# Optimization experiments

Hardware: AMD Instinct MI355X
Metric: run time of the kernel (lower is better)

## Reference

```python
import jax, jax.numpy as jnp
import numpy as np

N = 256   # events in the document
D = 768   # embed_dim
R = 7     # out_dim == num_relations (label 6 == NONE, filtered from graph)
H = 150   # Score hidden_dim


def _pair_idx(n):
    # torch ordering: [(i,k) for i in range(n) for k in range(n) if i != k]
    ii = np.repeat(np.arange(n), n)
    jj = np.tile(np.arange(n), n)
    m = ii != jj
    return jnp.asarray(ii[m], jnp.int32), jnp.asarray(jj[m], jnp.int32)


def _mlp(x, w1, b1, w2, b2, w3, b3):
    # Score module, eval mode (dropout off)
    h = jax.nn.relu(x @ w1 + b1)
    h = jax.nn.relu(h @ w2 + b2)
    return h @ w3 + b3


def _rgcn_conv(x, src, dst, etype, keep, w, root, bias):
    # PyG RGCNConv (num_bases=None, aggr='mean'):
    # out[i] = sum_r mean_{j in N_r(i)} x_j @ W_r + x_i @ root + bias
    # Linearity lets us aggregate x_j first, then apply W_r once per (node, rel).
    n, d = x.shape
    r = w.shape[0]
    seg = dst.astype(jnp.int32) * r + etype.astype(jnp.int32)      # [E]
    msg = x[src] * keep[:, None]                                   # [E, D]
    agg = jax.ops.segment_sum(msg, seg, num_segments=n * r)        # [N*R, D]
    cnt = jax.ops.segment_sum(keep, seg, num_segments=n * r)       # [N*R]
    mean = (agg / jnp.maximum(cnt, 1.0)[:, None]).reshape(n, r, d)
    return jnp.einsum('nrd,rde->ne', mean, w) + x @ root + bias


def setup_inputs():
    key = jax.random.key(0)
    ks = jax.random.split(key, 12)
    g = lambda k, s, sc=0.02: jax.random.normal(k, s, dtype=jnp.float32) * sc
    P = N * (N - 1)
    z = lambda s: jnp.zeros(s, jnp.float32)
    return {
        'embed': jax.random.normal(ks[0], (N, D), dtype=jnp.float32),
        'labels': jax.random.randint(ks[1], (P,), 0, R),
        'conv1_w': g(ks[2], (R, D, D)), 'conv1_root': g(ks[3], (D, D)), 'conv1_bias': z((D,)),
        'conv2_w': g(ks[4], (R, D, D)), 'conv2_root': g(ks[5], (D, D)), 'conv2_bias': z((D,)),
        'base_w1': g(ks[6], (2 * D, H)), 'base_b1': z((H,)),
        'base_w2': g(ks[7], (H, H)), 'base_b2': z((H,)),
        'base_w3': g(ks[8], (H, R)), 'base_b3': z((R,)),
        'cls_w1': g(ks[9], (2 * D, H)), 'cls_b1': z((H,)),
        'cls_w2': g(ks[10], (H, H)), 'cls_b2': z((H,)),
        'cls_w3': g(ks[11], (H, R)), 'cls_b3': z((R,)),
    }


def reference(embed, labels, conv1_w, conv1_root, conv1_bias,
              conv2_w, conv2_root, conv2_bias,
              base_w1, base_b1, base_w2, base_b2, base_w3, base_b3,
              cls_w1, cls_b1, cls_w2, cls_b2, cls_w3, cls_b3):
    n = embed.shape[0]
    src, dst = _pair_idx(n)                                        # all ordered pairs i != k

    # baseline scorer on raw-embedding pairs (frozen in torch; its argmax is unused)
    pairs0 = jnp.concatenate([embed[src], embed[dst]], axis=1)     # [P, 2D]
    _noise = _mlp(pairs0, base_w1, base_b1, base_w2, base_b2, base_w3, base_b3)

    # graph edges: keep only pairs whose label != 6 (NONE)
    keep = (labels != R - 1).astype(embed.dtype)                   # [P]
    etype = jnp.where(labels == R - 1, 0, labels)                  # dummy type, zero-weighted

    # RGCN (eval mode: dropout off)
    x = jax.nn.relu(_rgcn_conv(embed, src, dst, etype, keep, conv1_w, conv1_root, conv1_bias))
    out = _rgcn_conv(x, src, dst, etype, keep, conv2_w, conv2_root, conv2_bias)

    # classifier on RGCN-output pairs (full pair set again)
    pairs = jnp.concatenate([out[src], out[dst]], axis=1)          # [P, 2D]
    return _mlp(pairs, cls_w1, cls_b1, cls_w2, cls_b2, cls_w3, cls_b3)  # [P, 7]
```

## Files before the change

kernel.cpp:

```cpp
#include <hip/hip_runtime.h>

typedef unsigned short u16;
typedef unsigned int   u32;
typedef __attribute__((ext_vector_type(8))) short bf16x8;
typedef __attribute__((ext_vector_type(4))) float f32x4;

#define KCAT 5376

struct Params {
    const float* embed; const int* labels;
    const float* c1w; const float* c1root; const float* c1b;
    const float* c2w; const float* c2root; const float* c2b;
    const float* cw1; const float* cb1; const float* cw2;
    const float* cb2; const float* cw3; const float* cb3;
    u16* S; float* recip; u16* Acat1; u16* Acat2;
    u16* Pemb; u16* Px; u16* PW1; u16* PC1; u16* Pw2c; u16* Pw3;
    u16* W2C1p; float* cvec; float* AB; float* outp;
};

__device__ inline u16 f2bf(float f) {
    union { float f; u32 u; } v; v.f = f;
    u32 r = v.u + 0x7FFFu + ((v.u >> 16) & 1u);
    return (u16)(r >> 16);
}
__device__ inline f32x4 mfma16(bf16x8 a, bf16x8 b, f32x4 c) {
    return __builtin_amdgcn_mfma_f32_16x16x32_bf16(a, b, c, 0, 0, 0);
}

__device__ inline void pack_f32(const float* __restrict__ src, int ld, int rows, int cols,
                                u16* __restrict__ dst, int ntot, int kt0, int nt0,
                                int ntiles, int tile) {
    int ktile = tile / ntiles, ntile = tile % ntiles;
    int lane = threadIdx.x & 63;
    int m = lane & 15, hi = lane >> 4;
    int n = ntile * 16 + m;
    u16 tmp[8];
#pragma unroll
    for (int j = 0; j < 8; ++j) {
        int kk = ktile * 32 + hi * 8 + j;
        tmp[j] = (kk < rows && n < cols) ? f2bf(src[(size_t)kk * ld + n]) : (u16)0;
    }
    u16* d = dst + (((size_t)(kt0 + ktile) * ntot + (nt0 + ntile)) * 64 + lane) * 8;
    *(bf16x8*)d = *(const bf16x8*)tmp;
}

__device__ inline f32x4 gemm_tile(const u16* __restrict__ A, int lda,
                                  const u16* __restrict__ Bp,
                                  int row0, int nt, int ntot, int ktiles) {
    int lane = threadIdx.x & 63;
    int m = lane & 15, hi = lane >> 4;
    const u16* arow = A + (size_t)(row0 + m) * lda + hi * 8;
    const u16* bptr = Bp + ((size_t)nt * 64 + lane) * 8;
    f32x4 acc = {0.f, 0.f, 0.f, 0.f};
#pragma unroll 4
    for (int kt = 0; kt < ktiles; ++kt) {
        bf16x8 a = *(const bf16x8*)(arow + kt * 32);
        bf16x8 b = *(const bf16x8*)(bptr + (size_t)kt * ntot * 512);
        acc = mfma16(a, b, acc);
    }
    return acc;
}

__global__ __launch_bounds__(256) void kp0(Params p) {
    int w = threadIdx.x >> 6, lane = threadIdx.x & 63;
    int job = blockIdx.x * 4 + w;
    if (job < 256) {
        int k = job;
        int lab[4];
#pragma unroll
        for (int g = 0; g < 4; ++g) {
            int i = lane + g * 64;
            lab[g] = (i == k) ? -1 : p.labels[i * 255 + k - (k > i ? 1 : 0)];
        }
#pragma unroll
        for (int r = 0; r < 6; ++r) {
            int c = 0;
#pragma unroll
            for (int g = 0; g < 4; ++g) c += __popcll(__ballot(lab[g] == r));
#pragma unroll
            for (int g = 0; g < 4; ++g) {
                int i = lane + g * 64;
                p.S[(k * 6 + r) * 256 + i] = (lab[g] == r) ? (u16)0x3F80 : (u16)0;
            }
            if (lane == 0) p.recip[k * 6 + r] = 1.0f / (float)(c > 1 ? c : 1);
        }
    } else if (job < 640) {
        int idx = (job - 256) * 512 + lane * 8;
        int row = idx / 768, col = idx - row * 768;
        f32x4 a = *(const f32x4*)(p.embed + idx);
        f32x4 b = *(const f32x4*)(p.embed + idx + 4);
        u16 tmp[8];
#pragma unroll
        for (int e = 0; e < 4; ++e) { tmp[e] = f2bf(a[e]); tmp[e + 4] = f2bf(b[e]); }
        *(bf16x8*)(p.Acat1 + (size_t)row * KCAT + 4608 + col) = *(const bf16x8*)tmp;
    }
    else if (job < 1024) pack_f32(p.embed, 768, 256, 768, p.Pemb, 48, 0, 0, 48, job - 640);
    else if (job < 7936) pack_f32(p.c1w, 768, 4608, 768, p.PW1, 48, 0, 0, 48, job - 1024);
    else if (job < 9088) pack_f32(p.c1root, 768, 768, 768, p.PW1, 48, 144, 0, 48, job - 7936);
    else if (job < 9328) pack_f32(p.cw1, 150, 768, 150, p.PC1, 20, 0, 0, 10, job - 9088);
    else if (job < 9568) pack_f32(p.cw1 + 768 * 150, 150, 768, 150, p.PC1, 20, 0, 10, 10, job - 9328);
    else if (job < 9618) pack_f32(p.cw2, 150, 150, 150, p.Pw2c, 10, 0, 0, 10, job - 9568);
    else if (job < 9623) pack_f32(p.cw3, 7, 150, 7, p.Pw3, 1, 0, 0, 1, job - 9618);
}

__device__ void mean_tile(const Params& p, const u16* Bp, u16* Acat, int tile) {
    int rt = tile / 48, nt = tile % 48;
    f32x4 acc = gemm_tile(p.S, 256, Bp, rt * 16, nt, 48, 8);
    int lane = threadIdx.x & 63;
    int col = nt * 16 + (lane & 15), hi = lane >> 4;
#pragma unroll
    for (int r = 0; r < 4; ++r) {
        int g = rt * 16 + hi * 4 + r;
        float scale = p.recip[g];
        int node = g / 6, rel = g - node * 6;
        Acat[(size_t)node * KCAT + rel * 768 + col] = f2bf(acc[r] * scale);
    }
}

__device__ void w2c1_job(const Params& p, int q) {
    int lane = threadIdx.x & 63;
    int mtb = q / 5, ntb = q % 5;
    int m = lane & 15, hi = lane >> 4;
    int row0 = mtb * 32;
    f32x4 acc[2][4];
#pragma unroll
    for (int t = 0; t < 2; ++t)
#pragma unroll
        for (int qq = 0; qq < 4; ++qq) acc[t][qq] = {0.f, 0.f, 0.f, 0.f};
    for (int kt = 0; kt < 24; ++kt) {
        int e0 = kt * 32 + hi * 8;
        bf16x8 a[2];
#pragma unroll
        for (int t = 0; t < 2; ++t) {
            int r = row0 + t * 16 + m;
            const float* src = (r < 4608) ? (p.c2w + (size_t)r * 768)
                                          : (p.c2root + (size_t)(r - 4608) * 768);
            f32x4 x0 = *(const f32x4*)(src + e0);
            f32x4 x1 = *(const f32x4*)(src + e0 + 4);
            u16 tmp[8];
#pragma unroll
            for (int e = 0; e < 4; ++e) { tmp[e] = f2bf(x0[e]); tmp[e + 4] = f2bf(x1[e]); }
            a[t] = *(const bf16x8*)tmp;
        }
#pragma unroll
        for (int qq = 0; qq < 4; ++qq) {
            int nt = ntb * 4 + qq;
            bf16x8 b = *(const bf16x8*)(p.PC1 + ((size_t)(kt * 20 + nt) * 64 + lane) * 8);
            acc[0][qq] = mfma16(a[0], b, acc[0][qq]);
            acc[1][qq] = mfma16(a[1], b, acc[1][qq]);
        }
    }
#pragma unroll
    for (int t = 0; t < 2; ++t)
#pragma unroll
        for (int qq = 0; qq < 4; ++qq) {
            int nt = ntb * 4 + qq;
#pragma unroll
            for (int r4 = 0; r4 < 4; ++r4) {
                int kg = row0 + t * 16 + hi * 4 + r4;
                int kt2 = kg >> 5, j = kg & 7, hi2 = (kg >> 3) & 3;
                p.W2C1p[(((size_t)kt2 * 20 + nt) * 64 + hi2 * 16 + m) * 8 + j] = f2bf(acc[t][qq][r4]);
            }
        }
}

__device__ void cvec_job(const Params& p, int nt) {
    int lane = threadIdx.x & 63;
    int m = lane & 15, hi = lane >> 4;
    f32x4 acc = {0.f, 0.f, 0.f, 0.f};
    for (int kt = 0; kt < 24; ++kt) {
        int e0 = kt * 32 + hi * 8;
        f32x4 x0 = *(const f32x4*)(p.c2b + e0);
        f32x4 x1 = *(const f32x4*)(p.c2b + e0 + 4);
        u16 tmp[8];
#pragma unroll
        for (int e = 0; e < 4; ++e) {
            tmp[e]     = (m == 0) ? f2bf(x0[e]) : (u16)0;
            tmp[e + 4] = (m == 0) ? f2bf(x1[e]) : (u16)0;
        }
        bf16x8 a = *(const bf16x8*)tmp;
        bf16x8 b = *(const bf16x8*)(p.PC1 + ((size_t)(kt * 20 + nt) * 64 + lane) * 8);
        acc = mfma16(a, b, acc);
    }
    if (lane < 16) {
        int j = nt * 16 + lane;
        float bias = (j < 150) ? p.cb1[j] : 0.f;
        p.cvec[j] = acc[0] + bias;
    }
}

__global__ __launch_bounds__(256) void kp1(Params p) {
    int w = threadIdx.x >> 6;
    int job = blockIdx.x * 4 + w;
    if (job < 4608) mean_tile(p, p.Pemb, p.Acat1, job);
}

__global__ __launch_bounds__(256) void kp2(Params p) {
    __shared__ float red[4 * 64 * 4];
    int w = threadIdx.x >> 6, lane = threadIdx.x & 63;
    int b = blockIdx.x;
    if (b >= 768) {
        int job = (b - 768) * 4 + w;
        if (job < 840)      w2c1_job(p, job);
        else if (job < 860) cvec_job(p, job - 840);
        return;
    }
    int m = lane & 15, hi = lane >> 4;
    int rt = b / 48, nt = b % 48;
    const u16* arow = p.Acat1 + (size_t)(rt * 16 + m) * KCAT + hi * 8;
    const u16* bptr = p.PW1 + ((size_t)nt * 64 + lane) * 8;
    f32x4 acc = {0.f, 0.f, 0.f, 0.f};
#pragma unroll 4
    for (int kt = w * 42; kt < (w + 1) * 42; ++kt) {
        bf16x8 a = *(const bf16x8*)(arow + kt * 32);
        bf16x8 bb = *(const bf16x8*)(bptr + (size_t)kt * 48 * 512);
        acc = mfma16(a, bb, acc);
    }
    *(f32x4*)&red[(w * 64 + lane) * 4] = acc;
    __syncthreads();
    if (w == 0) {
        f32x4 s = *(f32x4*)&red[lane * 4];
#pragma unroll
        for (int ww = 1; ww < 4; ++ww) s += *(f32x4*)&red[(ww * 64 + lane) * 4];
        int col = nt * 16 + m;
        float bbv = p.c1b[col];
#pragma unroll
        for (int r = 0; r < 4; ++r) {
            int g = rt * 16 + hi * 4 + r;
            float v = fmaxf(s[r] + bbv, 0.f);
            u16 bv = f2bf(v);
            p.Acat2[(size_t)g * KCAT + 4608 + col] = bv;
            p.Px[(((size_t)(g >> 5) * 48 + nt) * 64 + (((g >> 3) & 3) * 16 + m)) * 8 + (g & 7)] = bv;
        }
    }
}

__global__ __launch_bounds__(256) void kp3(Params p) {
    int w = threadIdx.x >> 6;
    int job = blockIdx.x * 4 + w;
    if (job < 4608) mean_tile(p, p.Px, p.Acat2, job);
}

__global__ __launch_bounds__(256) void kp4(Params p) {
    __shared__ float red2[4 * 64 * 4];
    int w = threadIdx.x >> 6, lane = threadIdx.x & 63;
    int m = lane & 15, hi = lane >> 4;
    int b = blockIdx.x;
    int rt = b / 20, nt = b % 20;
    const u16* arow = p.Acat2 + (size_t)(rt * 16 + m) * KCAT + hi * 8;
    const u16* bptr = p.W2C1p + ((size_t)nt * 64 + lane) * 8;
    f32x4 acc = {0.f, 0.f, 0.f, 0.f};
#pragma unroll 4
    for (int kt = w * 42; kt < (w + 1) * 42; ++kt) {
        bf16x8 a = *(const bf16x8*)(arow + kt * 32);
        bf16x8 bb = *(const bf16x8*)(bptr + (size_t)kt * 20 * 512);
        acc = mfma16(a, bb, acc);
    }
    *(f32x4*)&red2[(w * 64 + lane) * 4] = acc;
    __syncthreads();
    if (w == 0) {
        f32x4 s = *(f32x4*)&red2[lane * 4];
#pragma unroll
        for (int ww = 1; ww < 4; ++ww) s += *(f32x4*)&red2[(ww * 64 + lane) * 4];
        int j = nt * 16 + m;
        float cv = p.cvec[j];
#pragma unroll
        for (int r = 0; r < 4; ++r) {
            int g = rt * 16 + hi * 4 + r;
            p.AB[(size_t)g * 320 + j] = s[r] + cv;
        }
    }
}

__global__ __launch_bounds__(256) void kp5(Params p) {
    __shared__ u16 h2t[4][16][168];
    int w = threadIdx.x >> 6, lane = threadIdx.x & 63;
    int m = lane & 15, hi = lane >> 4;
    int pb = blockIdx.x * 64 + w * 16;
    int pp = pb + m;
    int i = pp / 255, rem = pp - i * 255;
    int k = rem + (rem >= i ? 1 : 0);
    const float* Ar = p.AB + (size_t)i * 320;
    const float* Br = p.AB + (size_t)k * 320 + 160;

    bf16x8 af[5];
#pragma unroll
    for (int kk = 0; kk < 5; ++kk) {
        int c = kk * 32 + hi * 8;
        f32x4 a0 = *(const f32x4*)(Ar + c);
        f32x4 a1 = *(const f32x4*)(Ar + c + 4);
        f32x4 b0 = *(const f32x4*)(Br + c);
        f32x4 b1v = *(const f32x4*)(Br + c + 4);
        f32x4 s0 = a0 + b0, s1 = a1 + b1v;
        bf16x8 f;
#pragma unroll
        for (int e = 0; e < 4; ++e) {
            f[e]     = (short)f2bf(fmaxf(s0[e], 0.f));
            f[e + 4] = (short)f2bf(fmaxf(s1[e], 0.f));
        }
        af[kk] = f;
    }

#pragma unroll
    for (int nt = 0; nt < 10; ++nt) {
        f32x4 acc = {0.f, 0.f, 0.f, 0.f};
#pragma unroll
        for (int kk = 0; kk < 5; ++kk) {
            bf16x8 b = *(const bf16x8*)(p.Pw2c + ((size_t)(kk * 10 + nt) * 64 + lane) * 8);
            acc = mfma16(af[kk], b, acc);
        }
        int col = nt * 16 + m;
        float bb = (col < 150) ? p.cb2[col] : 0.f;
#pragma unroll
        for (int r = 0; r < 4; ++r) {
            float v = fmaxf(acc[r] + bb, 0.f);
            h2t[w][hi * 4 + r][col] = f2bf(v);
        }
    }
    __syncthreads();

    f32x4 acc3 = {0.f, 0.f, 0.f, 0.f};
#pragma unroll
    for (int kk = 0; kk < 5; ++kk) {
        bf16x8 a = *(const bf16x8*)(&h2t[w][m][kk * 32 + hi * 8]);
        bf16x8 b = *(const bf16x8*)(p.Pw3 + ((size_t)kk * 64 + lane) * 8);
        acc3 = mfma16(a, b, acc3);
    }
    if (m < 7) {
        float bb = p.cb3[m];
#pragma unroll
        for (int r = 0; r < 4; ++r) {
            int p2 = pb + hi * 4 + r;
            p.outp[p2 * 7 + m] = acc3[r] + bb;
        }
    }
}

extern "C" void kernel_launch(void* const* d_in, const int* in_sizes, int n_in,
                              void* d_out, int out_size, void* d_ws, size_t ws_size,
                              hipStream_t stream) {
    char* ws = (char*)d_ws;
    Params hp;
    hp.embed  = (const float*)d_in[0];
    hp.labels = (const int*)d_in[1];
    hp.c1w    = (const float*)d_in[2];
    hp.c1root = (const float*)d_in[3];
    hp.c1b    = (const float*)d_in[4];
    hp.c2w    = (const float*)d_in[5];
    hp.c2root = (const float*)d_in[6];
    hp.c2b    = (const float*)d_in[7];
    hp.cw1    = (const float*)d_in[14];
    hp.cb1    = (const float*)d_in[15];
    hp.cw2    = (const float*)d_in[16];
    hp.cb2    = (const float*)d_in[17];
    hp.cw3    = (const float*)d_in[18];
    hp.cb3    = (const float*)d_in[19];
    hp.S      = (u16*)(ws + 0);
    hp.recip  = (float*)(ws + 786432);
    hp.Acat1  = (u16*)(ws + 792576);
    hp.Acat2  = (u16*)(ws + 3545088);
    hp.Pemb   = (u16*)(ws + 6297600);
    hp.Px     = (u16*)(ws + 6690816);
    hp.PW1    = (u16*)(ws + 7084032);
    hp.PC1    = (u16*)(ws + 15341568);
    hp.Pw2c   = (u16*)(ws + 15833088);
    hp.Pw3    = (u16*)(ws + 15935488);
    hp.W2C1p  = (u16*)(ws + 15945728);
    hp.cvec   = (float*)(ws + 19386368);
    hp.AB     = (float*)(ws + 19387648);
    hp.outp   = (float*)d_out;

    kp0<<<2406, 256, 0, stream>>>(hp);
    kp1<<<1152, 256, 0, stream>>>(hp);
    kp2<<<983, 256, 0, stream>>>(hp);
    kp3<<<1152, 256, 0, stream>>>(hp);
    kp4<<<320, 256, 0, stream>>>(hp);
    kp5<<<1020, 256, 0, stream>>>(hp);
}
```

Before: 91.63 us.

## Compute first mean aggregation on the fly from fp32 embed, drop packed embed

Moves building the selection matrix into its own small kernel. The first-layer mean aggregation now reads fp32 embed directly with strided loads, converts to bf16 inside the loop, and runs inside the packing kernel, so the separate packed-embed buffer and the kp1 launch go away. The intent is to cut one launch and one round trip of packed data. In exchange, each wave does uncoalesced column-strided loads of embed, one scalar per lane per row.

```diff
diff --git a/kernel.cpp b/kernel.cpp
--- a/kernel.cpp
+++ b/kernel.cpp
@@ -14,7 +14,7 @@
     const float* cw1; const float* cb1; const float* cw2;
     const float* cb2; const float* cw3; const float* cb3;
     u16* S; float* recip; u16* Acat1; u16* Acat2;
-    u16* Pemb; u16* Px; u16* PW1; u16* PC1; u16* Pw2c; u16* Pw3;
+    u16* Px; u16* PW1; u16* PC1; u16* Pw2c; u16* Pw3;
     u16* W2C1p; float* cvec; float* AB; float* outp;
 };
 
@@ -61,31 +61,66 @@
     return acc;
 }
 
+__global__ __launch_bounds__(256) void kps(Params p) {
+    int w = threadIdx.x >> 6, lane = threadIdx.x & 63;
+    int job = blockIdx.x * 4 + w;
+    if (job >= 256) return;
+    int k = job;
+    int lab[4];
+#pragma unroll
+    for (int g = 0; g < 4; ++g) {
+        int i = lane + g * 64;
+        lab[g] = (i == k) ? -1 : p.labels[i * 255 + k - (k > i ? 1 : 0)];
+    }
+#pragma unroll
+    for (int r = 0; r < 6; ++r) {
+        int c = 0;
+#pragma unroll
+        for (int g = 0; g < 4; ++g) c += __popcll(__ballot(lab[g] == r));
+#pragma unroll
+        for (int g = 0; g < 4; ++g) {
+            int i = lane + g * 64;
+            p.S[(k * 6 + r) * 256 + i] = (lab[g] == r) ? (u16)0x3F80 : (u16)0;
+        }
+        if (lane == 0) p.recip[k * 6 + r] = 1.0f / (float)(c > 1 ? c : 1);
+    }
+}
+
+__device__ void mean1_otf(const Params& p, int tile) {
+    int rt = tile / 48, nt = tile % 48;
+    int lane = threadIdx.x & 63;
+    int m = lane & 15, hi = lane >> 4;
+    const u16* arow = p.S + (size_t)(rt * 16 + m) * 256 + hi * 8;
+    const float* bcol = p.embed + nt * 16 + m;
+    f32x4 acc = {0.f, 0.f, 0.f, 0.f};
+#pragma unroll 2
+    for (int kt = 0; kt < 8; ++kt) {
+        bf16x8 a = *(const bf16x8*)(arow + kt * 32);
+        int k0 = kt * 32 + hi * 8;
+        u16 tmp[8];
+#pragma unroll
+        for (int j = 0; j < 8; ++j)
+            tmp[j] = f2bf(bcol[(size_t)(k0 + j) * 768]);
+        bf16x8 b = *(const bf16x8*)tmp;
+        acc = mfma16(a, b, acc);
+    }
+    int col = nt * 16 + m;
+#pragma unroll
+    for (int r = 0; r < 4; ++r) {
+        int g = rt * 16 + hi * 4 + r;
+        float scale = p.recip[g];
+        int node = g / 6, rel = g - node * 6;
+        p.Acat1[(size_t)node * KCAT + rel * 768 + col] = f2bf(acc[r] * scale);
+    }
+}
+
 __global__ __launch_bounds__(256) void kp0(Params p) {
     int w = threadIdx.x >> 6, lane = threadIdx.x & 63;
     int job = blockIdx.x * 4 + w;
-    if (job < 256) {
-        int k = job;
-        int lab[4];
-#pragma unroll
-        for (int g = 0; g < 4; ++g) {
-            int i = lane + g * 64;
-            lab[g] = (i == k) ? -1 : p.labels[i * 255 + k - (k > i ? 1 : 0)];
-        }
-#pragma unroll
-        for (int r = 0; r < 6; ++r) {
-            int c = 0;
-#pragma unroll
-            for (int g = 0; g < 4; ++g) c += __popcll(__ballot(lab[g] == r));
-#pragma unroll
-            for (int g = 0; g < 4; ++g) {
-                int i = lane + g * 64;
-                p.S[(k * 6 + r) * 256 + i] = (lab[g] == r) ? (u16)0x3F80 : (u16)0;
-            }
-            if (lane == 0) p.recip[k * 6 + r] = 1.0f / (float)(c > 1 ? c : 1);
-        }
-    } else if (job < 640) {
-        int idx = (job - 256) * 512 + lane * 8;
+    if (job < 4608) {
+        mean1_otf(p, job);
+    } else if (job < 4992) {
+        int idx = (job - 4608) * 512 + lane * 8;
         int row = idx / 768, col = idx - row * 768;
         f32x4 a = *(const f32x4*)(p.embed + idx);
         f32x4 b = *(const f32x4*)(p.embed + idx + 4);
@@ -94,13 +129,12 @@
         for (int e = 0; e < 4; ++e) { tmp[e] = f2bf(a[e]); tmp[e + 4] = f2bf(b[e]); }
         *(bf16x8*)(p.Acat1 + (size_t)row * KCAT + 4608 + col) = *(const bf16x8*)tmp;
     }
-    else if (job < 1024) pack_f32(p.embed, 768, 256, 768, p.Pemb, 48, 0, 0, 48, job - 640);
-    else if (job < 7936) pack_f32(p.c1w, 768, 4608, 768, p.PW1, 48, 0, 0, 48, job - 1024);
-    else if (job < 9088) pack_f32(p.c1root, 768, 768, 768, p.PW1, 48, 144, 0, 48, job - 7936);
-    else if (job < 9328) pack_f32(p.cw1, 150, 768, 150, p.PC1, 20, 0, 0, 10, job - 9088);
-    else if (job < 9568) pack_f32(p.cw1 + 768 * 150, 150, 768, 150, p.PC1, 20, 0, 10, 10, job - 9328);
-    else if (job < 9618) pack_f32(p.cw2, 150, 150, 150, p.Pw2c, 10, 0, 0, 10, job - 9568);
-    else if (job < 9623) pack_f32(p.cw3, 7, 150, 7, p.Pw3, 1, 0, 0, 1, job - 9618);
+    else if (job < 11904) pack_f32(p.c1w, 768, 4608, 768, p.PW1, 48, 0, 0, 48, job - 4992);
+    else if (job < 13056) pack_f32(p.c1root, 768, 768, 768, p.PW1, 48, 144, 0, 48, job - 11904);
+    else if (job < 13296) pack_f32(p.cw1, 150, 768, 150, p.PC1, 20, 0, 0, 10, job - 13056);
+    else if (job < 13536) pack_f32(p.cw1 + 768 * 150, 150, 768, 150, p.PC1, 20, 0, 10, 10, job - 13296);
+    else if (job < 13586) pack_f32(p.cw2, 150, 150, 150, p.Pw2c, 10, 0, 0, 10, job - 13536);
+    else if (job < 13591) pack_f32(p.cw3, 7, 150, 7, p.Pw3, 1, 0, 0, 1, job - 13586);
 }
 
 __device__ void mean_tile(const Params& p, const u16* Bp, u16* Acat, int tile) {
@@ -187,12 +221,6 @@
         float bias = (j < 150) ? p.cb1[j] : 0.f;
         p.cvec[j] = acc[0] + bias;
     }
-}
-
-__global__ __launch_bounds__(256) void kp1(Params p) {
-    int w = threadIdx.x >> 6;
-    int job = blockIdx.x * 4 + w;
-    if (job < 4608) mean_tile(p, p.Pemb, p.Acat1, job);
 }
 
 __global__ __launch_bounds__(256) void kp2(Params p) {
@@ -359,7 +387,6 @@
     hp.recip  = (float*)(ws + 786432);
     hp.Acat1  = (u16*)(ws + 792576);
     hp.Acat2  = (u16*)(ws + 3545088);
-    hp.Pemb   = (u16*)(ws + 6297600);
     hp.Px     = (u16*)(ws + 6690816);
     hp.PW1    = (u16*)(ws + 7084032);
     hp.PC1    = (u16*)(ws + 15341568);
@@ -370,8 +397,8 @@
     hp.AB     = (float*)(ws + 19387648);
     hp.outp   = (float*)d_out;
 
-    kp0<<<2406, 256, 0, stream>>>(hp);
-    kp1<<<1152, 256, 0, stream>>>(hp);
+    kps<<<64, 256, 0, stream>>>(hp);
+    kp0<<<3398, 256, 0, stream>>>(hp);
     kp2<<<983, 256, 0, stream>>>(hp);
     kp3<<<1152, 256, 0, stream>>>(hp);
     kp4<<<320, 256, 0, stream>>>(hp);
```

Result: slower. 94.13 us (+2.7%).
